# Performance work log

Hardware: AMD Instinct MI355X
Metric: run time of the kernel (lower is better)

The kernel has to match this reference:

```python
import jax, jax.numpy as jnp
import numpy as np

B, N, H = 8, 256, 128
EPS = 1e-5

def setup_inputs() -> dict:
    key = jax.random.key(0)
    ks = jax.random.split(key, 16)
    s = 1.0 / np.sqrt(H)
    inp = {
        "x": jax.random.normal(ks[0], (B, N, H), jnp.float32),
        "e": jax.random.normal(ks[1], (B, N, N, H), jnp.float32),
        # EdgeFeatures: U, V linear layers
        "Ue_w": jax.random.normal(ks[2], (H, H), jnp.float32) * s,
        "Ue_b": jax.random.normal(ks[3], (H,), jnp.float32) * s,
        "Ve_w": jax.random.normal(ks[4], (H, H), jnp.float32) * s,
        "Ve_b": jax.random.normal(ks[5], (H,), jnp.float32) * s,
        # NodeFeatures: U, V linear layers
        "Un_w": jax.random.normal(ks[6], (H, H), jnp.float32) * s,
        "Un_b": jax.random.normal(ks[7], (H,), jnp.float32) * s,
        "Vn_w": jax.random.normal(ks[8], (H, H), jnp.float32) * s,
        "Vn_b": jax.random.normal(ks[9], (H,), jnp.float32) * s,
        # BatchNorm affine params (track_running_stats=False -> batch stats)
        "bne_w": jnp.ones((H,), jnp.float32),
        "bne_b": jnp.zeros((H,), jnp.float32),
        "bnn_w": jnp.ones((H,), jnp.float32),
        "bnn_b": jnp.zeros((H,), jnp.float32),
    }
    return inp

def _bn(t, axes, w, b):
    # BatchNorm with batch statistics (biased variance), per-channel over last dim
    m = jnp.mean(t, axis=axes, keepdims=True)
    v = jnp.var(t, axis=axes, keepdims=True)
    return (t - m) * jax.lax.rsqrt(v + EPS) * w + b

def reference(x, e, Ue_w, Ue_b, Ve_w, Ve_b, Un_w, Un_b, Vn_w, Vn_b,
              bne_w, bne_b, bnn_w, bnn_b):
    # EdgeFeatures: e_new = U(e) + V(x)_i + V(x)_j  -> [B,N,N,H]
    Vx = x @ Ve_w.T + Ve_b                              # [B,N,H]
    e_new = e @ Ue_w.T + Ue_b + Vx[:, :, None, :] + Vx[:, None, :, :]
    gate = jax.nn.sigmoid(e_new)                        # [B,N,N,H]
    # NodeFeatures (aggregation='sum'): Ux + sum_j gate_ij * Vn(x)_j
    Vnx = x @ Vn_w.T + Vn_b                             # [B,N,H]
    agg = jnp.sum(gate * Vnx[:, None, :, :], axis=2)    # [B,N,H]
    x_new = x @ Un_w.T + Un_b + agg
    # BatchNorm (batch stats) + ReLU + residual
    e_bn = _bn(e_new, (0, 1, 2), bne_w, bne_b)
    x_bn = _bn(x_new, (0, 1), bnn_w, bnn_b)
    return x + jax.nn.relu(x_bn), e + jax.nn.relu(e_bn)
```

## Files before the change

kernel.cpp:

```cpp
#include <hip/hip_runtime.h>
#include <cstdint>
#include <cstddef>


typedef float  f4v  __attribute__((ext_vector_type(4)));
typedef short  s8v  __attribute__((ext_vector_type(8)));

__device__ __forceinline__ unsigned short f2bf(float x) {
    unsigned u = __builtin_bit_cast(unsigned, x);
    u = (u + 0x7FFFu + ((u >> 16) & 1u)) >> 16;
    return (unsigned short)u;
}

__device__ __forceinline__ float sigmoid_f(float v) {
    float e = exp2f(-1.44269504088896f * v);
    return __builtin_amdgcn_rcpf(1.0f + e);
}

__global__ __launch_bounds__(256) void k0_proj(
    const float* __restrict__ x,
    const float* __restrict__ Ve_w, const float* __restrict__ Ve_b,
    const float* __restrict__ Vn_w, const float* __restrict__ Vn_b,
    const float* __restrict__ Un_w, const float* __restrict__ Un_b,
    float* __restrict__ ws)
{
    int bid = blockIdx.x;
    int m = bid >> 8;
    int rbase = (bid & 255) * 8;
    int tid = threadIdx.x;
    int h = tid & 127;
    int lr = tid >> 7;

    const float* W; const float* bb; float* out;
    if (m == 0)      { W = Ve_w; bb = Ve_b; out = ws; }
    else if (m == 1) { W = Vn_w; bb = Vn_b; out = ws + 262144; }
    else             { W = Un_w; bb = Un_b; out = ws + 524288; }

    __shared__ __align__(16) float xs[8][128];
    for (int idx = tid; idx < 1024; idx += 256)
        xs[idx >> 7][idx & 127] = x[(rbase + (idx >> 7)) * 128 + (idx & 127)];

    if (bid == 0) {
        ws[1048576 + tid] = 0.0f;
        ws[1048576 + 256 + tid] = 0.0f;
    }
    __syncthreads();

    float acc[4] = {0.f, 0.f, 0.f, 0.f};
    float bv = bb[h];
    const float4* Wr = (const float4*)(W + h * 128);
    for (int k4 = 0; k4 < 32; ++k4) {
        float4 w4 = Wr[k4];
        int k = k4 * 4;
        #pragma unroll
        for (int q = 0; q < 4; ++q) {
            int rl = lr * 4 + q;
            acc[q] += w4.x * xs[rl][k] + w4.y * xs[rl][k + 1]
                    + w4.z * xs[rl][k + 2] + w4.w * xs[rl][k + 3];
        }
    }
    #pragma unroll
    for (int q = 0; q < 4; ++q)
        out[(rbase + lr * 4 + q) * 128 + h] = acc[q] + bv;
}

__global__ __launch_bounds__(256, 4) void k1_stats(
    const float* __restrict__ e,
    const float* __restrict__ Ue_w, const float* __restrict__ Ue_b,
    float* __restrict__ ws)
{
    const float* Vx  = ws;
    const float* Vnx = ws + 262144;
    const float* Ux  = ws + 524288;
    float* agg    = ws + 786432;
    float* esum   = ws + 1048576;
    float* esumsq = ws + 1048704;
    float* nsum   = ws + 1048832;
    float* nsumsq = ws + 1048960;

    int bid = blockIdx.x;
    int b = bid >> 8;
    int tid = threadIdx.x;
    int wave = tid >> 6;
    int lane = tid & 63;
    int col  = lane & 15;
    int quad = lane >> 4;

    __shared__ __align__(16) unsigned short Wl[128 * 136];
    __shared__ __align__(16) unsigned short Al[16 * 136];
    __shared__ float addi[128];

    for (int t = tid * 8; t < 16384; t += 2048) {
        int row = t >> 7, c = t & 127;
        const float4* src = (const float4*)(Ue_w + t);
        float4 v0 = src[0], v1 = src[1];
        s8v pk;
        pk[0] = (short)f2bf(v0.x); pk[1] = (short)f2bf(v0.y);
        pk[2] = (short)f2bf(v0.z); pk[3] = (short)f2bf(v0.w);
        pk[4] = (short)f2bf(v1.x); pk[5] = (short)f2bf(v1.y);
        pk[6] = (short)f2bf(v1.z); pk[7] = (short)f2bf(v1.w);
        *(s8v*)(&Wl[row * 136 + c]) = pk;
    }
    if (tid < 128) addi[tid] = Ue_b[tid] + Vx[bid * 128 + tid];
    __syncthreads();

    float sum0 = 0.f, sum1 = 0.f, ss0 = 0.f, ss1 = 0.f, ag0 = 0.f, ag1 = 0.f;
    int h0 = wave * 32 + col;
    int h1 = h0 + 16;

    const int arow = tid >> 4, akb = (tid & 15) * 8;
    const float* eblk = e + (size_t)bid * 32768;

    for (int jt = 0; jt < 16; ++jt) {
        int jbase = jt * 16;
        {
            const float4* src = (const float4*)(eblk + (jbase + arow) * 128 + akb);
            float4 v0 = src[0], v1 = src[1];
            s8v pk;
            pk[0] = (short)f2bf(v0.x); pk[1] = (short)f2bf(v0.y);
            pk[2] = (short)f2bf(v0.z); pk[3] = (short)f2bf(v0.w);
            pk[4] = (short)f2bf(v1.x); pk[5] = (short)f2bf(v1.y);
            pk[6] = (short)f2bf(v1.z); pk[7] = (short)f2bf(v1.w);
            *(s8v*)(&Al[arow * 136 + akb]) = pk;
        }
        __syncthreads();

        f4v acc0 = {0.f, 0.f, 0.f, 0.f}, acc1 = {0.f, 0.f, 0.f, 0.f};
        #pragma unroll
        for (int kk = 0; kk < 4; ++kk) {
            int ko = kk * 32 + quad * 8;
            s8v a  = *(const s8v*)(&Al[col * 136 + ko]);
            s8v b0 = *(const s8v*)(&Wl[h0 * 136 + ko]);
            s8v b1 = *(const s8v*)(&Wl[h1 * 136 + ko]);
            acc0 = __builtin_amdgcn_mfma_f32_16x16x32_bf16(a, b0, acc0, 0, 0, 0);
            acc1 = __builtin_amdgcn_mfma_f32_16x16x32_bf16(a, b1, acc1, 0, 0, 0);
        }
        float ai0 = addi[h0], ai1 = addi[h1];
        #pragma unroll
        for (int r = 0; r < 4; ++r) {
            int j = jbase + quad * 4 + r;
            const float* vxr = Vx  + ((b << 8) + j) * 128;
            const float* vnr = Vnx + ((b << 8) + j) * 128;
            float v0 = acc0[r] + ai0 + vxr[h0];
            float v1 = acc1[r] + ai1 + vxr[h1];
            sum0 += v0; ss0 += v0 * v0;
            sum1 += v1; ss1 += v1 * v1;
            ag0 += sigmoid_f(v0) * vnr[h0];
            ag1 += sigmoid_f(v1) * vnr[h1];
        }
        __syncthreads();
    }

    sum0 += __shfl_xor(sum0, 16); sum0 += __shfl_xor(sum0, 32);
    sum1 += __shfl_xor(sum1, 16); sum1 += __shfl_xor(sum1, 32);
    ss0  += __shfl_xor(ss0, 16);  ss0  += __shfl_xor(ss0, 32);
    ss1  += __shfl_xor(ss1, 16);  ss1  += __shfl_xor(ss1, 32);
    ag0  += __shfl_xor(ag0, 16);  ag0  += __shfl_xor(ag0, 32);
    ag1  += __shfl_xor(ag1, 16);  ag1  += __shfl_xor(ag1, 32);

    if (lane < 16) {
        atomicAdd(&esum[h0], sum0);
        atomicAdd(&esumsq[h0], ss0);
        atomicAdd(&esum[h1], sum1);
        atomicAdd(&esumsq[h1], ss1);
        agg[bid * 128 + h0] = ag0;
        agg[bid * 128 + h1] = ag1;
        float v0 = Ux[bid * 128 + h0] + ag0;
        float v1 = Ux[bid * 128 + h1] + ag1;
        atomicAdd(&nsum[h0], v0);
        atomicAdd(&nsumsq[h0], v0 * v0);
        atomicAdd(&nsum[h1], v1);
        atomicAdd(&nsumsq[h1], v1 * v1);
    }
}

__global__ __launch_bounds__(128) void k15_finalize(
    const float* __restrict__ bne_w, const float* __restrict__ bne_b,
    const float* __restrict__ bnn_w, const float* __restrict__ bnn_b,
    float* __restrict__ ws)
{
    int tid = threadIdx.x;
    const float* esum   = ws + 1048576;
    const float* esumsq = ws + 1048704;
    const float* nsum   = ws + 1048832;
    const float* nsumsq = ws + 1048960;
    float* esc = ws + 1049088;  float* esh = ws + 1049216;
    float* nsc = ws + 1049344;  float* nsh = ws + 1049472;

    {
        float m = esum[tid] * (1.0f / 524288.0f);
        float q = esumsq[tid] * (1.0f / 524288.0f);
        float var = q - m * m;
        float rs = rsqrtf(var + 1e-5f);
        float sc = rs * bne_w[tid];
        esc[tid] = sc;
        esh[tid] = bne_b[tid] - m * sc;
    }
    {
        float m = nsum[tid] * (1.0f / 2048.0f);
        float q = nsumsq[tid] * (1.0f / 2048.0f);
        float var = q - m * m;
        float rs = rsqrtf(var + 1e-5f);
        float sc = rs * bnn_w[tid];
        nsc[tid] = sc;
        nsh[tid] = bnn_b[tid] - m * sc;
    }
}

__global__ __launch_bounds__(256, 3) void k2_apply(
    const float* __restrict__ e,
    const float* __restrict__ x,
    const float* __restrict__ Ue_w, const float* __restrict__ Ue_b,
    const float* __restrict__ ws, float* __restrict__ out_x,
    float* __restrict__ out_e)
{
    const float* Vx  = ws;
    const float* Ux  = ws + 524288;
    const float* agg = ws + 786432;
    const float* esc = ws + 1049088;
    const float* esh = ws + 1049216;
    const float* nsc = ws + 1049344;
    const float* nsh = ws + 1049472;

    int bid = blockIdx.x;
    int b = bid >> 8;
    int tid = threadIdx.x;
    int wave = tid >> 6;
    int lane = tid & 63;
    int col  = lane & 15;
    int quad = lane >> 4;

    __shared__ __align__(16) unsigned short Wl[128 * 136];
    __shared__ __align__(16) float Af[16 * 132];
    __shared__ __align__(16) float Ot[16 * 132];
    __shared__ float addi[128], escl[128], eshl[128];

    if (tid < 128) {
        float v = Ux[bid * 128 + tid] + agg[bid * 128 + tid];
        float bn = v * nsc[tid] + nsh[tid];
        out_x[bid * 128 + tid] = x[bid * 128 + tid] + fmaxf(bn, 0.0f);
    }

    for (int t = tid * 8; t < 16384; t += 2048) {
        int row = t >> 7, c = t & 127;
        const float4* src = (const float4*)(Ue_w + t);
        float4 v0 = src[0], v1 = src[1];
        s8v pk;
        pk[0] = (short)f2bf(v0.x); pk[1] = (short)f2bf(v0.y);
        pk[2] = (short)f2bf(v0.z); pk[3] = (short)f2bf(v0.w);
        pk[4] = (short)f2bf(v1.x); pk[5] = (short)f2bf(v1.y);
        pk[6] = (short)f2bf(v1.z); pk[7] = (short)f2bf(v1.w);
        *(s8v*)(&Wl[row * 136 + c]) = pk;
    }
    if (tid < 128) {
        addi[tid] = Ue_b[tid] + Vx[bid * 128 + tid];
        escl[tid] = esc[tid];
        eshl[tid] = esh[tid];
    }
    __syncthreads();

    const int arow = tid >> 4, akb = (tid & 15) * 8;
    const float* eblk = e + (size_t)bid * 32768;
    float* oblk = out_e + (size_t)bid * 32768;
    int h0 = wave * 32 + col;
    int h1 = h0 + 16;

    for (int jt = 0; jt < 16; ++jt) {
        int jbase = jt * 16;
        {
            const float4* src = (const float4*)(eblk + (jbase + arow) * 128 + akb);
            float4 v0 = src[0], v1 = src[1];
            *(float4*)(&Af[arow * 132 + akb])     = v0;
            *(float4*)(&Af[arow * 132 + akb + 4]) = v1;
        }
        __syncthreads();

        f4v acc0 = {0.f, 0.f, 0.f, 0.f}, acc1 = {0.f, 0.f, 0.f, 0.f};
        #pragma unroll
        for (int kk = 0; kk < 4; ++kk) {
            int ko = kk * 32 + quad * 8;
            const float* ap = &Af[col * 132 + ko];
            float4 p0 = *(const float4*)ap;
            float4 p1 = *(const float4*)(ap + 4);
            s8v a;
            a[0] = (short)f2bf(p0.x); a[1] = (short)f2bf(p0.y);
            a[2] = (short)f2bf(p0.z); a[3] = (short)f2bf(p0.w);
            a[4] = (short)f2bf(p1.x); a[5] = (short)f2bf(p1.y);
            a[6] = (short)f2bf(p1.z); a[7] = (short)f2bf(p1.w);
            s8v b0 = *(const s8v*)(&Wl[h0 * 136 + ko]);
            s8v b1 = *(const s8v*)(&Wl[h1 * 136 + ko]);
            acc0 = __builtin_amdgcn_mfma_f32_16x16x32_bf16(a, b0, acc0, 0, 0, 0);
            acc1 = __builtin_amdgcn_mfma_f32_16x16x32_bf16(a, b1, acc1, 0, 0, 0);
        }
        float ai0 = addi[h0], ai1 = addi[h1];
        float sc0 = escl[h0], sv0 = eshl[h0];
        float sc1 = escl[h1], sv1 = eshl[h1];
        #pragma unroll
        for (int r = 0; r < 4; ++r) {
            int jl = quad * 4 + r;
            int j = jbase + jl;
            const float* vxr = Vx + ((b << 8) + j) * 128;
            float v0 = acc0[r] + ai0 + vxr[h0];
            float v1 = acc1[r] + ai1 + vxr[h1];
            float r0 = fmaxf(v0 * sc0 + sv0, 0.0f);
            float r1 = fmaxf(v1 * sc1 + sv1, 0.0f);
            Ot[jl * 132 + h0] = Af[jl * 132 + h0] + r0;
            Ot[jl * 132 + h1] = Af[jl * 132 + h1] + r1;
        }
        __syncthreads();

        {
            float4 o0 = *(const float4*)(&Ot[arow * 132 + akb]);
            float4 o1 = *(const float4*)(&Ot[arow * 132 + akb + 4]);
            float4* dst = (float4*)(oblk + (jbase + arow) * 128 + akb);
            dst[0] = o0; dst[1] = o1;
        }
    }
}

extern "C" void kernel_launch(void* const* d_in, const int* in_sizes, int n_in,
                              void* d_out, int out_size, void* d_ws, size_t ws_size,
                              hipStream_t stream)
{
    const float* x     = (const float*)d_in[0];
    const float* e     = (const float*)d_in[1];
    const float* Ue_w  = (const float*)d_in[2];
    const float* Ue_b  = (const float*)d_in[3];
    const float* Ve_w  = (const float*)d_in[4];
    const float* Ve_b  = (const float*)d_in[5];
    const float* Un_w  = (const float*)d_in[6];
    const float* Un_b  = (const float*)d_in[7];
    const float* Vn_w  = (const float*)d_in[8];
    const float* Vn_b  = (const float*)d_in[9];
    const float* bne_w = (const float*)d_in[10];
    const float* bne_b = (const float*)d_in[11];
    const float* bnn_w = (const float*)d_in[12];
    const float* bnn_b = (const float*)d_in[13];
    float* ws    = (float*)d_ws;
    float* out_x = (float*)d_out;
    float* out_e = (float*)d_out + 262144;

    hipLaunchKernelGGL(k0_proj, dim3(768), dim3(256), 0, stream,
                       x, Ve_w, Ve_b, Vn_w, Vn_b, Un_w, Un_b, ws);
    hipLaunchKernelGGL(k1_stats, dim3(2048), dim3(256), 0, stream,
                       e, Ue_w, Ue_b, ws);
    hipLaunchKernelGGL(k15_finalize, dim3(1), dim3(128), 0, stream,
                       bne_w, bne_b, bnn_w, bnn_b, ws);
    hipLaunchKernelGGL(k2_apply, dim3(2048), dim3(256), 0, stream,
                       e, x, Ue_w, Ue_b, ws, out_x, out_e);
}
```

Before: 612.6 us.

## Precast Ue_w to bf16 once, keep weights in registers, double-buffer e tiles

Ue_w is converted to bf16 once in extra blocks of the projection kernel and stored in the workspace. The stats and apply kernels now keep each lane's weight fragments in registers instead of reconverting the whole matrix into LDS in every block. Both kernels process 32-row tiles with register prefetch of the next e tile into a double-buffered LDS area. The finalize kernel is folded into the apply kernel, which now writes out_e directly from global e instead of staging through LDS, reducing LDS use and raising occupancy. The risk is the uncoalesced per-element out_e stores and e re-reads in the apply kernel.

```diff
diff --git a/kernel.cpp b/kernel.cpp
--- a/kernel.cpp
+++ b/kernel.cpp
@@ -22,12 +22,33 @@
     const float* __restrict__ Ve_w, const float* __restrict__ Ve_b,
     const float* __restrict__ Vn_w, const float* __restrict__ Vn_b,
     const float* __restrict__ Un_w, const float* __restrict__ Un_b,
+    const float* __restrict__ Ue_w,
     float* __restrict__ ws)
 {
     int bid = blockIdx.x;
+    int tid = threadIdx.x;
+
+    if (bid >= 768) {
+        int g = (bid - 768) * 256 + tid;
+        const float4* src = (const float4*)(Ue_w + g * 16);
+        unsigned short* Wbf = (unsigned short*)(ws + 1049600);
+        float4 v0 = src[0], v1 = src[1], v2 = src[2], v3 = src[3];
+        s8v p0, p1;
+        p0[0] = (short)f2bf(v0.x); p0[1] = (short)f2bf(v0.y);
+        p0[2] = (short)f2bf(v0.z); p0[3] = (short)f2bf(v0.w);
+        p0[4] = (short)f2bf(v1.x); p0[5] = (short)f2bf(v1.y);
+        p0[6] = (short)f2bf(v1.z); p0[7] = (short)f2bf(v1.w);
+        p1[0] = (short)f2bf(v2.x); p1[1] = (short)f2bf(v2.y);
+        p1[2] = (short)f2bf(v2.z); p1[3] = (short)f2bf(v2.w);
+        p1[4] = (short)f2bf(v3.x); p1[5] = (short)f2bf(v3.y);
+        p1[6] = (short)f2bf(v3.z); p1[7] = (short)f2bf(v3.w);
+        *(s8v*)(Wbf + g * 16)     = p0;
+        *(s8v*)(Wbf + g * 16 + 8) = p1;
+        return;
+    }
+
     int m = bid >> 8;
     int rbase = (bid & 255) * 8;
-    int tid = threadIdx.x;
     int h = tid & 127;
     int lr = tid >> 7;
 
@@ -66,7 +87,7 @@
 
 __global__ __launch_bounds__(256, 4) void k1_stats(
     const float* __restrict__ e,
-    const float* __restrict__ Ue_w, const float* __restrict__ Ue_b,
+    const float* __restrict__ Ue_b,
     float* __restrict__ ws)
 {
     const float* Vx  = ws;
@@ -77,6 +98,7 @@
     float* esumsq = ws + 1048704;
     float* nsum   = ws + 1048832;
     float* nsumsq = ws + 1048960;
+    const unsigned short* Wbf = (const unsigned short*)(ws + 1049600);
 
     int bid = blockIdx.x;
     int b = bid >> 8;
@@ -85,70 +107,80 @@
     int lane = tid & 63;
     int col  = lane & 15;
     int quad = lane >> 4;
-
-    __shared__ __align__(16) unsigned short Wl[128 * 136];
-    __shared__ __align__(16) unsigned short Al[16 * 136];
-    __shared__ float addi[128];
-
-    for (int t = tid * 8; t < 16384; t += 2048) {
-        int row = t >> 7, c = t & 127;
-        const float4* src = (const float4*)(Ue_w + t);
-        float4 v0 = src[0], v1 = src[1];
-        s8v pk;
-        pk[0] = (short)f2bf(v0.x); pk[1] = (short)f2bf(v0.y);
-        pk[2] = (short)f2bf(v0.z); pk[3] = (short)f2bf(v0.w);
-        pk[4] = (short)f2bf(v1.x); pk[5] = (short)f2bf(v1.y);
-        pk[6] = (short)f2bf(v1.z); pk[7] = (short)f2bf(v1.w);
-        *(s8v*)(&Wl[row * 136 + c]) = pk;
-    }
-    if (tid < 128) addi[tid] = Ue_b[tid] + Vx[bid * 128 + tid];
-    __syncthreads();
-
-    float sum0 = 0.f, sum1 = 0.f, ss0 = 0.f, ss1 = 0.f, ag0 = 0.f, ag1 = 0.f;
     int h0 = wave * 32 + col;
     int h1 = h0 + 16;
 
-    const int arow = tid >> 4, akb = (tid & 15) * 8;
+    __shared__ __align__(16) unsigned short Al[2][32 * 136];
+    __shared__ float addi[128];
+
+    if (tid < 128) addi[tid] = Ue_b[tid] + Vx[bid * 128 + tid];
+
+    s8v wf0[4], wf1[4];
+    #pragma unroll
+    for (int kk = 0; kk < 4; ++kk) {
+        wf0[kk] = *(const s8v*)(Wbf + h0 * 128 + kk * 32 + quad * 8);
+        wf1[kk] = *(const s8v*)(Wbf + h1 * 128 + kk * 32 + quad * 8);
+    }
+
+    const int arow = tid >> 4;
+    const int akb  = (tid & 15) * 8;
     const float* eblk = e + (size_t)bid * 32768;
 
-    for (int jt = 0; jt < 16; ++jt) {
-        int jbase = jt * 16;
+    float4 pv0, pv1, pv2, pv3;
+    {
+        const float4* s0 = (const float4*)(eblk + arow * 128 + akb);
+        const float4* s1 = (const float4*)(eblk + (arow + 16) * 128 + akb);
+        pv0 = s0[0]; pv1 = s0[1]; pv2 = s1[0]; pv3 = s1[1];
+    }
+
+    float sum0 = 0.f, sum1 = 0.f, ss0 = 0.f, ss1 = 0.f, ag0 = 0.f, ag1 = 0.f;
+
+    for (int jt = 0; jt < 8; ++jt) {
+        unsigned short* Ac = &Al[jt & 1][0];
         {
-            const float4* src = (const float4*)(eblk + (jbase + arow) * 128 + akb);
-            float4 v0 = src[0], v1 = src[1];
-            s8v pk;
-            pk[0] = (short)f2bf(v0.x); pk[1] = (short)f2bf(v0.y);
-            pk[2] = (short)f2bf(v0.z); pk[3] = (short)f2bf(v0.w);
-            pk[4] = (short)f2bf(v1.x); pk[5] = (short)f2bf(v1.y);
-            pk[6] = (short)f2bf(v1.z); pk[7] = (short)f2bf(v1.w);
-            *(s8v*)(&Al[arow * 136 + akb]) = pk;
-        }
-        __syncthreads();
-
-        f4v acc0 = {0.f, 0.f, 0.f, 0.f}, acc1 = {0.f, 0.f, 0.f, 0.f};
+            s8v pa, pb;
+            pa[0] = (short)f2bf(pv0.x); pa[1] = (short)f2bf(pv0.y);
+            pa[2] = (short)f2bf(pv0.z); pa[3] = (short)f2bf(pv0.w);
+            pa[4] = (short)f2bf(pv1.x); pa[5] = (short)f2bf(pv1.y);
+            pa[6] = (short)f2bf(pv1.z); pa[7] = (short)f2bf(pv1.w);
+            pb[0] = (short)f2bf(pv2.x); pb[1] = (short)f2bf(pv2.y);
+            pb[2] = (short)f2bf(pv2.z); pb[3] = (short)f2bf(pv2.w);
+            pb[4] = (short)f2bf(pv3.x); pb[5] = (short)f2bf(pv3.y);
+            pb[6] = (short)f2bf(pv3.z); pb[7] = (short)f2bf(pv3.w);
+            *(s8v*)(&Ac[arow * 136 + akb])        = pa;
+            *(s8v*)(&Ac[(arow + 16) * 136 + akb]) = pb;
+        }
+        if (jt < 7) {
+            const float4* s0 = (const float4*)(eblk + ((jt + 1) * 32 + arow) * 128 + akb);
+            const float4* s1 = (const float4*)(eblk + ((jt + 1) * 32 + arow + 16) * 128 + akb);
+            pv0 = s0[0]; pv1 = s0[1]; pv2 = s1[0]; pv3 = s1[1];
+        }
+        asm volatile("s_waitcnt lgkmcnt(0)" ::: "memory");
+        __builtin_amdgcn_s_barrier();
+
         #pragma unroll
-        for (int kk = 0; kk < 4; ++kk) {
-            int ko = kk * 32 + quad * 8;
-            s8v a  = *(const s8v*)(&Al[col * 136 + ko]);
-            s8v b0 = *(const s8v*)(&Wl[h0 * 136 + ko]);
-            s8v b1 = *(const s8v*)(&Wl[h1 * 136 + ko]);
-            acc0 = __builtin_amdgcn_mfma_f32_16x16x32_bf16(a, b0, acc0, 0, 0, 0);
-            acc1 = __builtin_amdgcn_mfma_f32_16x16x32_bf16(a, b1, acc1, 0, 0, 0);
-        }
-        float ai0 = addi[h0], ai1 = addi[h1];
-        #pragma unroll
-        for (int r = 0; r < 4; ++r) {
-            int j = jbase + quad * 4 + r;
-            const float* vxr = Vx  + ((b << 8) + j) * 128;
-            const float* vnr = Vnx + ((b << 8) + j) * 128;
-            float v0 = acc0[r] + ai0 + vxr[h0];
-            float v1 = acc1[r] + ai1 + vxr[h1];
-            sum0 += v0; ss0 += v0 * v0;
-            sum1 += v1; ss1 += v1 * v1;
-            ag0 += sigmoid_f(v0) * vnr[h0];
-            ag1 += sigmoid_f(v1) * vnr[h1];
-        }
-        __syncthreads();
+        for (int js = 0; js < 2; ++js) {
+            f4v acc0 = {0.f, 0.f, 0.f, 0.f}, acc1 = {0.f, 0.f, 0.f, 0.f};
+            #pragma unroll
+            for (int kk = 0; kk < 4; ++kk) {
+                s8v a = *(const s8v*)(&Ac[(js * 16 + col) * 136 + kk * 32 + quad * 8]);
+                acc0 = __builtin_amdgcn_mfma_f32_16x16x32_bf16(a, wf0[kk], acc0, 0, 0, 0);
+                acc1 = __builtin_amdgcn_mfma_f32_16x16x32_bf16(a, wf1[kk], acc1, 0, 0, 0);
+            }
+            float ai0 = addi[h0], ai1 = addi[h1];
+            #pragma unroll
+            for (int r = 0; r < 4; ++r) {
+                int j = jt * 32 + js * 16 + quad * 4 + r;
+                const float* vxr = Vx  + (size_t)((b << 8) + j) * 128;
+                const float* vnr = Vnx + (size_t)((b << 8) + j) * 128;
+                float v0 = acc0[r] + ai0 + vxr[h0];
+                float v1 = acc1[r] + ai1 + vxr[h1];
+                sum0 += v0; ss0 += v0 * v0;
+                sum1 += v1; ss1 += v1 * v1;
+                ag0 += sigmoid_f(v0) * vnr[h0];
+                ag1 += sigmoid_f(v1) * vnr[h1];
+            }
+        }
     }
 
     sum0 += __shfl_xor(sum0, 16); sum0 += __shfl_xor(sum0, 32);
@@ -174,53 +206,23 @@
     }
 }
 
-__global__ __launch_bounds__(128) void k15_finalize(
+__global__ __launch_bounds__(256, 4) void k2_apply(
+    const float* __restrict__ e,
+    const float* __restrict__ x,
+    const float* __restrict__ Ue_b,
     const float* __restrict__ bne_w, const float* __restrict__ bne_b,
     const float* __restrict__ bnn_w, const float* __restrict__ bnn_b,
-    float* __restrict__ ws)
-{
-    int tid = threadIdx.x;
-    const float* esum   = ws + 1048576;
-    const float* esumsq = ws + 1048704;
-    const float* nsum   = ws + 1048832;
-    const float* nsumsq = ws + 1048960;
-    float* esc = ws + 1049088;  float* esh = ws + 1049216;
-    float* nsc = ws + 1049344;  float* nsh = ws + 1049472;
-
-    {
-        float m = esum[tid] * (1.0f / 524288.0f);
-        float q = esumsq[tid] * (1.0f / 524288.0f);
-        float var = q - m * m;
-        float rs = rsqrtf(var + 1e-5f);
-        float sc = rs * bne_w[tid];
-        esc[tid] = sc;
-        esh[tid] = bne_b[tid] - m * sc;
-    }
-    {
-        float m = nsum[tid] * (1.0f / 2048.0f);
-        float q = nsumsq[tid] * (1.0f / 2048.0f);
-        float var = q - m * m;
-        float rs = rsqrtf(var + 1e-5f);
-        float sc = rs * bnn_w[tid];
-        nsc[tid] = sc;
-        nsh[tid] = bnn_b[tid] - m * sc;
-    }
-}
-
-__global__ __launch_bounds__(256, 3) void k2_apply(
-    const float* __restrict__ e,
-    const float* __restrict__ x,
-    const float* __restrict__ Ue_w, const float* __restrict__ Ue_b,
     const float* __restrict__ ws, float* __restrict__ out_x,
     float* __restrict__ out_e)
 {
-    const float* Vx  = ws;
-    const float* Ux  = ws + 524288;
-    const float* agg = ws + 786432;
-    const float* esc = ws + 1049088;
-    const float* esh = ws + 1049216;
-    const float* nsc = ws + 1049344;
-    const float* nsh = ws + 1049472;
+    const float* Vx   = ws;
+    const float* Ux   = ws + 524288;
+    const float* agg  = ws + 786432;
+    const float* esum = ws + 1048576;
+    const float* esumsq = ws + 1048704;
+    const float* nsum = ws + 1048832;
+    const float* nsumsq = ws + 1048960;
+    const unsigned short* Wbf = (const unsigned short*)(ws + 1049600);
 
     int bid = blockIdx.x;
     int b = bid >> 8;
@@ -229,91 +231,95 @@
     int lane = tid & 63;
     int col  = lane & 15;
     int quad = lane >> 4;
-
-    __shared__ __align__(16) unsigned short Wl[128 * 136];
-    __shared__ __align__(16) float Af[16 * 132];
-    __shared__ __align__(16) float Ot[16 * 132];
+    int h0 = wave * 32 + col;
+    int h1 = h0 + 16;
+
+    __shared__ __align__(16) unsigned short Al[2][32 * 136];
     __shared__ float addi[128], escl[128], eshl[128];
 
     if (tid < 128) {
+        float m  = esum[tid]   * (1.0f / 524288.0f);
+        float q  = esumsq[tid] * (1.0f / 524288.0f);
+        float rs = rsqrtf(q - m * m + 1e-5f);
+        float sc = rs * bne_w[tid];
+        escl[tid] = sc;
+        eshl[tid] = bne_b[tid] - m * sc;
+        addi[tid] = Ue_b[tid] + Vx[bid * 128 + tid];
+
+        float mn  = nsum[tid]   * (1.0f / 2048.0f);
+        float qn  = nsumsq[tid] * (1.0f / 2048.0f);
+        float rsn = rsqrtf(qn - mn * mn + 1e-5f);
+        float scn = rsn * bnn_w[tid];
+        float shn = bnn_b[tid] - mn * scn;
         float v = Ux[bid * 128 + tid] + agg[bid * 128 + tid];
-        float bn = v * nsc[tid] + nsh[tid];
-        out_x[bid * 128 + tid] = x[bid * 128 + tid] + fmaxf(bn, 0.0f);
-    }
-
-    for (int t = tid * 8; t < 16384; t += 2048) {
-        int row = t >> 7, c = t & 127;
-        const float4* src = (const float4*)(Ue_w + t);
-        float4 v0 = src[0], v1 = src[1];
-        s8v pk;
-        pk[0] = (short)f2bf(v0.x); pk[1] = (short)f2bf(v0.y);
-        pk[2] = (short)f2bf(v0.z); pk[3] = (short)f2bf(v0.w);
-        pk[4] = (short)f2bf(v1.x); pk[5] = (short)f2bf(v1.y);
-        pk[6] = (short)f2bf(v1.z); pk[7] = (short)f2bf(v1.w);
-        *(s8v*)(&Wl[row * 136 + c]) = pk;
-    }
-    if (tid < 128) {
-        addi[tid] = Ue_b[tid] + Vx[bid * 128 + tid];
-        escl[tid] = esc[tid];
-        eshl[tid] = esh[tid];
-    }
-    __syncthreads();
-
-    const int arow = tid >> 4, akb = (tid & 15) * 8;
+        out_x[bid * 128 + tid] = x[bid * 128 + tid] + fmaxf(v * scn + shn, 0.0f);
+    }
+
+    s8v wf0[4], wf1[4];
+    #pragma unroll
+    for (int kk = 0; kk < 4; ++kk) {
+        wf0[kk] = *(const s8v*)(Wbf + h0 * 128 + kk * 32 + quad * 8);
+        wf1[kk] = *(const s8v*)(Wbf + h1 * 128 + kk * 32 + quad * 8);
+    }
+
+    const int arow = tid >> 4;
+    const int akb  = (tid & 15) * 8;
     const float* eblk = e + (size_t)bid * 32768;
     float* oblk = out_e + (size_t)bid * 32768;
-    int h0 = wave * 32 + col;
-    int h1 = h0 + 16;
-
-    for (int jt = 0; jt < 16; ++jt) {
-        int jbase = jt * 16;
+
+    float4 pv0, pv1, pv2, pv3;
+    {
+        const float4* s0 = (const float4*)(eblk + arow * 128 + akb);
+        const float4* s1 = (const float4*)(eblk + (arow + 16) * 128 + akb);
+        pv0 = s0[0]; pv1 = s0[1]; pv2 = s1[0]; pv3 = s1[1];
+    }
+
+    for (int jt = 0; jt < 8; ++jt) {
+        unsigned short* Ac = &Al[jt & 1][0];
         {
-            const float4* src = (const float4*)(eblk + (jbase + arow) * 128 + akb);
-            float4 v0 = src[0], v1 = src[1];
-            *(float4*)(&Af[arow * 132 + akb])     = v0;
-            *(float4*)(&Af[arow * 132 + akb + 4]) = v1;
-        }
-        __syncthreads();
-
-        f4v acc0 = {0.f, 0.f, 0.f, 0.f}, acc1 = {0.f, 0.f, 0.f, 0.f};
+            s8v pa, pb;
+            pa[0] = (short)f2bf(pv0.x); pa[1] = (short)f2bf(pv0.y);
+            pa[2] = (short)f2bf(pv0.z); pa[3] = (short)f2bf(pv0.w);
+            pa[4] = (short)f2bf(pv1.x); pa[5] = (short)f2bf(pv1.y);
+            pa[6] = (short)f2bf(pv1.z); pa[7] = (short)f2bf(pv1.w);
+            pb[0] = (short)f2bf(pv2.x); pb[1] = (short)f2bf(pv2.y);
+            pb[2] = (short)f2bf(pv2.z); pb[3] = (short)f2bf(pv2.w);
+            pb[4] = (short)f2bf(pv3.x); pb[5] = (short)f2bf(pv3.y);
+            pb[6] = (short)f2bf(pv3.z); pb[7] = (short)f2bf(pv3.w);
+            *(s8v*)(&Ac[arow * 136 + akb])        = pa;
+            *(s8v*)(&Ac[(arow + 16) * 136 + akb]) = pb;
+        }
+        if (jt < 7) {
+            const float4* s0 = (const float4*)(eblk + ((jt + 1) * 32 + arow) * 128 + akb);
+            const float4* s1 = (const float4*)(eblk + ((jt + 1) * 32 + arow + 16) * 128 + akb);
+            pv0 = s0[0]; pv1 = s0[1]; pv2 = s1[0]; pv3 = s1[1];
+        }
+        asm volatile("s_waitcnt lgkmcnt(0)" ::: "memory");
+        __builtin_amdgcn_s_barrier();
+
         #pragma unroll
-        for (int kk = 0; kk < 4; ++kk) {
-            int ko = kk * 32 + quad * 8;
-            const float* ap = &Af[col * 132 + ko];
-            float4 p0 = *(const float4*)ap;
-            float4 p1 = *(const float4*)(ap + 4);
-            s8v a;
-            a[0] = (short)f2bf(p0.x); a[1] = (short)f2bf(p0.y);
-            a[2] = (short)f2bf(p0.z); a[3] = (short)f2bf(p0.w);
-            a[4] = (short)f2bf(p1.x); a[5] = (short)f2bf(p1.y);
-            a[6] = (short)f2bf(p1.z); a[7] = (short)f2bf(p1.w);
-            s8v b0 = *(const s8v*)(&Wl[h0 * 136 + ko]);
-            s8v b1 = *(const s8v*)(&Wl[h1 * 136 + ko]);
-            acc0 = __builtin_amdgcn_mfma_f32_16x16x32_bf16(a, b0, acc0, 0, 0, 0);
-            acc1 = __builtin_amdgcn_mfma_f32_16x16x32_bf16(a, b1, acc1, 0, 0, 0);
-        }
-        float ai0 = addi[h0], ai1 = addi[h1];
-        float sc0 = escl[h0], sv0 = eshl[h0];
-        float sc1 = escl[h1], sv1 = eshl[h1];
-        #pragma unroll
-        for (int r = 0; r < 4; ++r) {
-            int jl = quad * 4 + r;
-            int j = jbase + jl;
-            const float* vxr = Vx + ((b << 8) + j) * 128;
-            float v0 = acc0[r] + ai0 + vxr[h0];
-            float v1 = acc1[r] + ai1 + vxr[h1];
-            float r0 = fmaxf(v0 * sc0 + sv0, 0.0f);
-            float r1 = fmaxf(v1 * sc1 + sv1, 0.0f);
-            Ot[jl * 132 + h0] = Af[jl * 132 + h0] + r0;
-            Ot[jl * 132 + h1] = Af[jl * 132 + h1] + r1;
-        }
-        __syncthreads();
-
-        {
-            float4 o0 = *(const float4*)(&Ot[arow * 132 + akb]);
-            float4 o1 = *(const float4*)(&Ot[arow * 132 + akb + 4]);
-            float4* dst = (float4*)(oblk + (jbase + arow) * 128 + akb);
-            dst[0] = o0; dst[1] = o1;
+        for (int js = 0; js < 2; ++js) {
+            f4v acc0 = {0.f, 0.f, 0.f, 0.f}, acc1 = {0.f, 0.f, 0.f, 0.f};
+            #pragma unroll
+            for (int kk = 0; kk < 4; ++kk) {
+                s8v a = *(const s8v*)(&Ac[(js * 16 + col) * 136 + kk * 32 + quad * 8]);
+                acc0 = __builtin_amdgcn_mfma_f32_16x16x32_bf16(a, wf0[kk], acc0, 0, 0, 0);
+                acc1 = __builtin_amdgcn_mfma_f32_16x16x32_bf16(a, wf1[kk], acc1, 0, 0, 0);
+            }
+            float ai0 = addi[h0], ai1 = addi[h1];
+            float sc0 = escl[h0], sh0 = eshl[h0];
+            float sc1 = escl[h1], sh1 = eshl[h1];
+            #pragma unroll
+            for (int r = 0; r < 4; ++r) {
+                int j = jt * 32 + js * 16 + quad * 4 + r;
+                const float* vxr = Vx + (size_t)((b << 8) + j) * 128;
+                float v0 = acc0[r] + ai0 + vxr[h0];
+                float v1 = acc1[r] + ai1 + vxr[h1];
+                float r0 = fmaxf(v0 * sc0 + sh0, 0.0f);
+                float r1 = fmaxf(v1 * sc1 + sh1, 0.0f);
+                oblk[j * 128 + h0] = eblk[j * 128 + h0] + r0;
+                oblk[j * 128 + h1] = eblk[j * 128 + h1] + r1;
+            }
         }
     }
 }
@@ -340,12 +346,10 @@
     float* out_x = (float*)d_out;
     float* out_e = (float*)d_out + 262144;
 
-    hipLaunchKernelGGL(k0_proj, dim3(768), dim3(256), 0, stream,
-                       x, Ve_w, Ve_b, Vn_w, Vn_b, Un_w, Un_b, ws);
+    hipLaunchKernelGGL(k0_proj, dim3(772), dim3(256), 0, stream,
+                       x, Ve_w, Ve_b, Vn_w, Vn_b, Un_w, Un_b, Ue_w, ws);
     hipLaunchKernelGGL(k1_stats, dim3(2048), dim3(256), 0, stream,
-                       e, Ue_w, Ue_b, ws);
-    hipLaunchKernelGGL(k15_finalize, dim3(1), dim3(128), 0, stream,
-                       bne_w, bne_b, bnn_w, bnn_b, ws);
+                       e, Ue_b, ws);
     hipLaunchKernelGGL(k2_apply, dim3(2048), dim3(256), 0, stream,
-                       e, x, Ue_w, Ue_b, ws, out_x, out_e);
-}
+                       e, x, Ue_b, bne_w, bne_b, bnn_w, bnn_b, ws, out_x, out_e);
+}
```

After: 583.0 us. 4.8% less time.
